# Kernel tuning notes

Measured on AMD Instinct MI355X. Metric: run time of the kernel, lower is better.

## Reference

```python
import jax, jax.numpy as jnp
import numpy as np

M, K, N = 4096, 7168, 18432  # tokens, in_features, out_features


def setup_inputs() -> dict:
    key = jax.random.key(0)
    kx, kw, ks = jax.random.split(key, 3)
    x = jax.random.normal(kx, (M, K), dtype=jnp.float32)
    # int8 quantized weight, layout [in_features, out_features] as in the torch module
    weight = jax.random.randint(kw, (K, N), -128, 128, dtype=jnp.int8)
    # per-output-channel dequant scale (bf16 in the original; fp32 here for a stable baseline)
    scale = jax.random.uniform(ks, (N,), dtype=jnp.float32) * 0.02 + 1e-3
    return {"x": x, "weight": weight, "scale": scale}


def reference(x, weight, scale):
    # Fused dequant + GEMM: y = x @ (int8_weight * scale_per_out_channel)
    w = weight.astype(x.dtype) * scale.astype(x.dtype)[None, :]  # [K, N]
    return x @ w  # [M, N]
```

## Files before the change

### kernel.cpp

```cpp
#include <hip/hip_runtime.h>
#include <hip/hip_bf16.h>
#include <cstdint>
#include <cstddef>

#define M_ 4096
#define K_ 7168
#define N_ 18432
#define NT 56

typedef __attribute__((ext_vector_type(4))) int i32x4;

#define AS1 __attribute__((address_space(1)))
#define AS3 __attribute__((address_space(3)))

__device__ __forceinline__ void gld_lds16(void* lds, const void* g) {
  __builtin_amdgcn_global_load_lds((const AS1 void*)g, (AS3 void*)lds, 16, 0, 0);
}

__global__ __launch_bounds__(256) void quant_x_kernel(const float* __restrict__ x,
                                                      signed char* __restrict__ xq,
                                                      float* __restrict__ sx) {
  const int m = blockIdx.x;
  const float4* row4 = (const float4*)(x + (size_t)m * K_);
  float mx = 0.f;
  for (int i = threadIdx.x; i < K_ / 4; i += 256) {
    float4 v = row4[i];
    mx = fmaxf(mx, fmaxf(fmaxf(fabsf(v.x), fabsf(v.y)), fmaxf(fabsf(v.z), fabsf(v.w))));
  }
#pragma unroll
  for (int d = 1; d < 64; d <<= 1) mx = fmaxf(mx, __shfl_xor(mx, d));
  __shared__ float wred[4];
  if ((threadIdx.x & 63) == 0) wred[threadIdx.x >> 6] = mx;
  __syncthreads();
  mx = fmaxf(fmaxf(wred[0], wred[1]), fmaxf(wred[2], wred[3]));
  const float inv = mx > 0.f ? 127.f / mx : 0.f;
  if (threadIdx.x == 0) sx[m] = mx / 127.f;
  char4* q4 = (char4*)(xq + (size_t)m * K_);
  for (int i = threadIdx.x; i < K_ / 4; i += 256) {
    float4 v = row4[i];
    char4 c;
    c.x = (signed char)__float2int_rn(v.x * inv);
    c.y = (signed char)__float2int_rn(v.y * inv);
    c.z = (signed char)__float2int_rn(v.z * inv);
    c.w = (signed char)__float2int_rn(v.w * inv);
    q4[i] = c;
  }
}

__global__ __launch_bounds__(256) void transpose_w_kernel(const int* __restrict__ W,
                                                          signed char* __restrict__ Wt) {
  __shared__ __align__(16) signed char t[64][80];
  const int k0 = blockIdx.x * 64;
  const int n0 = blockIdx.y * 64;
  const int r = threadIdx.x >> 4;
  const int c4 = (threadIdx.x & 15) * 4;
#pragma unroll
  for (int rr = 0; rr < 4; ++rr) {
    const int row = rr * 16 + r;
    int4 v = *(const int4*)(W + (size_t)(k0 + row) * N_ + n0 + c4);
    t[c4 + 0][row] = (signed char)v.x;
    t[c4 + 1][row] = (signed char)v.y;
    t[c4 + 2][row] = (signed char)v.z;
    t[c4 + 3][row] = (signed char)v.w;
  }
  __syncthreads();
  const int nr = threadIdx.x >> 2;
  const int cb = (threadIdx.x & 3) * 16;
  int4 o = *(const int4*)&t[nr][cb];
  *(int4*)(Wt + (size_t)(n0 + nr) * K_ + k0 + cb) = o;
}

__global__ __launch_bounds__(512, 2) void gemm_i8_kernel(const signed char* __restrict__ Aq,
                                                         const signed char* __restrict__ Bt,
                                                         const float* __restrict__ sx,
                                                         const float* __restrict__ scale,
                                                         float* __restrict__ C) {
  __shared__ __align__(16) signed char lds[131072];

  const int bid = blockIdx.x;
  const int xcd = bid & 7;
  const int j = bid >> 3;
  const int m0 = (j & 15) * 256;
  const int n0 = (xcd * 9 + (j >> 4)) * 256;

  const int tid = threadIdx.x;
  const int w = tid >> 6;
  const int lane = tid & 63;
  const int wr = w >> 2;
  const int wc = w & 3;

  const int fr = lane & 15;
  const int q = lane >> 4;
  const int sl = ((q ^ ((fr >> 1) & 3)) << 4);

  const int ls16 = (((lane & 3) ^ ((lane >> 3) & 3)) << 4);
  const int pr0 = w * 16 + (lane >> 2);
  const unsigned offA0 = (unsigned)(m0 + pr0) * K_ + ls16;
  const unsigned offA1 = (unsigned)(m0 + 128 + pr0) * K_ + ls16;
  const unsigned offB0 = (unsigned)(n0 + pr0) * K_ + ls16;
  const unsigned offB1 = (unsigned)(n0 + 128 + pr0) * K_ + ls16;

#define STAGE_A(T, KS) do {                                                        \
    const int tc_ = (T) < NT ? (T) : NT - 1;                                       \
    signed char* d_ = lds + (((T) & 1) * 32768 + (KS) * 16384 + w * 1024);         \
    gld_lds16(d_, Aq + (size_t)offA0 + tc_ * 128 + (KS) * 64);                     \
    gld_lds16(d_ + 8192, Aq + (size_t)offA1 + tc_ * 128 + (KS) * 64);              \
  } while (0)
#define STAGE_B(T, KS) do {                                                        \
    const int tc_ = (T) < NT ? (T) : NT - 1;                                       \
    signed char* d_ = lds + (65536 + ((T) & 1) * 32768 + (KS) * 16384 + w * 1024); \
    gld_lds16(d_, Bt + (size_t)offB0 + tc_ * 128 + (KS) * 64);                     \
    gld_lds16(d_ + 8192, Bt + (size_t)offB1 + tc_ * 128 + (KS) * 64);              \
  } while (0)
#define LDALL(BUF, KS) do {                                                        \
    const signed char* bb = lds + (65536 + (BUF) * 32768 + (KS) * 16384);          \
    const signed char* ab = lds + ((BUF) * 32768 + (KS) * 16384);                  \
    _Pragma("unroll") for (int n_ = 0; n_ < 4; ++n_)                               \
      fb[n_] = *(const i32x4*)(bb + (wc * 64 + n_ * 16 + fr) * 64 + sl);           \
    _Pragma("unroll") for (int f_ = 0; f_ < 8; ++f_)                               \
      fa[f_] = *(const i32x4*)(ab + (wr * 128 + f_ * 16 + fr) * 64 + sl);          \
  } while (0)
#define MFMA32 do {                                                                \
    __builtin_amdgcn_s_setprio(1);                                                 \
    _Pragma("unroll") for (int f_ = 0; f_ < 8; ++f_)                               \
    _Pragma("unroll") for (int n_ = 0; n_ < 4; ++n_)                               \
      acc[f_][n_] = __builtin_amdgcn_mfma_i32_16x16x64_i8(                         \
          fa[f_], fb[n_], acc[f_][n_], 0, 0, 0);                                   \
    __builtin_amdgcn_s_setprio(0);                                                 \
  } while (0)
#define BARRIER do { asm volatile("" ::: "memory");                                \
                     __builtin_amdgcn_s_barrier();                                 \
                     asm volatile("" ::: "memory"); } while (0)
#define WAIT00 asm volatile("s_waitcnt vmcnt(0) lgkmcnt(0)" ::: "memory")
#define VM8 asm volatile("s_waitcnt vmcnt(8)" ::: "memory")

#define KTILE(P, T_STAGE) do {                                                     \
    LDALL(P, 0);                                                                   \
    MFMA32;                                                                        \
    LDALL(P, 1);                                                                   \
    MFMA32;                                                                        \
    WAIT00;           \
    BARRIER;          \
    STAGE_A(T_STAGE, 0); STAGE_B(T_STAGE, 0);                                      \
    STAGE_A(T_STAGE, 1); STAGE_B(T_STAGE, 1);                                      \
  } while (0)

  i32x4 acc[8][4] = {};
  i32x4 fa[8], fb[4];

  STAGE_A(0, 0); STAGE_B(0, 0); STAGE_A(0, 1); STAGE_B(0, 1);
  STAGE_A(1, 0); STAGE_B(1, 0); STAGE_A(1, 1); STAGE_B(1, 1);
  VM8;
  BARRIER;

  for (int it = 0; it < NT / 2; ++it) {
    const int u = 2 * it;
    KTILE(0, u + 2);
    KTILE(1, u + 3);
  }

  const int mb = m0 + wr * 128;
  const int nb = n0 + wc * 64;
  const int col = lane & 15;
  const int rq = (lane >> 4) * 4;
  float scl[4];
#pragma unroll
  for (int n = 0; n < 4; ++n) scl[n] = scale[nb + n * 16 + col];
#pragma unroll
  for (int m = 0; m < 8; ++m) {
#pragma unroll
    for (int r = 0; r < 4; ++r) {
      const int row = mb + m * 16 + rq + r;
      const float s = sx[row];
      float* out = C + (size_t)row * N_ + nb + col;
#pragma unroll
      for (int n = 0; n < 4; ++n) out[n * 16] = (float)acc[m][n][r] * s * scl[n];
    }
  }
#undef STAGE_A
#undef STAGE_B
#undef LDALL
#undef MFMA32
#undef BARRIER
#undef WAIT00
#undef VM8
#undef KTILE
}

__global__ __launch_bounds__(256) void fb_gemm_kernel(const float* __restrict__ X,
                                                      const int* __restrict__ W,
                                                      const float* __restrict__ scale,
                                                      float* __restrict__ Y) {
  __shared__ float xs[16][65];
  __shared__ float ws_[16][65];
  const int bn = blockIdx.x * 64;
  const int bm = blockIdx.y * 64;
  const int tx = threadIdx.x & 15;
  const int ty = threadIdx.x >> 4;
  float acc[4][4] = {};
  for (int k0 = 0; k0 < K_; k0 += 16) {
    for (int i = threadIdx.x; i < 64 * 16; i += 256) {
      int r = i >> 4, c = i & 15;
      xs[c][r] = X[(size_t)(bm + r) * K_ + k0 + c];
    }
    for (int i = threadIdx.x; i < 16 * 64; i += 256) {
      int r = i >> 6, c = i & 63;
      ws_[r][c] = (float)W[(size_t)(k0 + r) * N_ + bn + c];
    }
    __syncthreads();
#pragma unroll
    for (int kk = 0; kk < 16; ++kk) {
      float a[4], b[4];
#pragma unroll
      for (int i = 0; i < 4; ++i) a[i] = xs[kk][ty * 4 + i];
#pragma unroll
      for (int j = 0; j < 4; ++j) b[j] = ws_[kk][tx * 4 + j];
#pragma unroll
      for (int i = 0; i < 4; ++i)
#pragma unroll
        for (int j = 0; j < 4; ++j) acc[i][j] += a[i] * b[j];
    }
    __syncthreads();
  }
#pragma unroll
  for (int i = 0; i < 4; ++i)
#pragma unroll
    for (int j = 0; j < 4; ++j)
      Y[(size_t)(bm + ty * 4 + i) * N_ + bn + tx * 4 + j] = acc[i][j] * scale[bn + tx * 4 + j];
}

extern "C" void kernel_launch(void* const* d_in, const int* in_sizes, int n_in,
                              void* d_out, int out_size, void* d_ws, size_t ws_size,
                              hipStream_t stream) {
  const float* x = (const float*)d_in[0];
  const int* w = (const int*)d_in[1];
  const float* scale = (const float*)d_in[2];
  float* y = (float*)d_out;

  const size_t xq_bytes = (size_t)M_ * K_;
  const size_t sx_off = xq_bytes;
  const size_t wt_off = sx_off + (size_t)M_ * 4;
  const size_t need = wt_off + (size_t)N_ * K_;

  if (ws_size >= need) {
    signed char* xq = (signed char*)d_ws;
    float* sx = (float*)((char*)d_ws + sx_off);
    signed char* wt = (signed char*)((char*)d_ws + wt_off);
    hipLaunchKernelGGL(quant_x_kernel, dim3(M_), dim3(256), 0, stream, x, xq, sx);
    hipLaunchKernelGGL(transpose_w_kernel, dim3(K_ / 64, N_ / 64), dim3(256), 0, stream, w, wt);
    hipLaunchKernelGGL(gemm_i8_kernel, dim3((M_ / 256) * (N_ / 256)), dim3(512), 0, stream,
                       xq, wt, sx, scale, y);
  } else {
    hipLaunchKernelGGL(fb_gemm_kernel, dim3(N_ / 64, M_ / 64), dim3(256), 0, stream,
                       x, w, scale, y);
  }
}
```

Before: 768.9 us.

## Switch int8 GEMM to 32x32x32 MFMA with register double-buffered fragment loads

```diff
diff --git a/kernel.cpp b/kernel.cpp
--- a/kernel.cpp
+++ b/kernel.cpp
@@ -9,6 +9,7 @@
 #define NT 56
 
 typedef __attribute__((ext_vector_type(4))) int i32x4;
+typedef __attribute__((ext_vector_type(16))) int i32x16;
 
 #define AS1 __attribute__((address_space(1)))
 #define AS3 __attribute__((address_space(3)))
@@ -89,9 +90,13 @@
   const int wr = w >> 2;
   const int wc = w & 3;
 
-  const int fr = lane & 15;
-  const int q = lane >> 4;
-  const int sl = ((q ^ ((fr >> 1) & 3)) << 4);
+  const int fr32 = lane & 31;
+  const int kh = lane >> 5;
+  const int sw = (fr32 >> 1) & 3;
+  const int ps0 = ((kh ^ sw) << 4);
+  const int ps1 = ps0 ^ 0x20;
+  const int rA = (wr * 128 + fr32) * 64;
+  const int rB = 65536 + (wc * 64 + fr32) * 64;
 
   const int ls16 = (((lane & 3) ^ ((lane >> 3) & 3)) << 4);
   const int pr0 = w * 16 + (lane >> 2);
@@ -112,46 +117,49 @@
     gld_lds16(d_, Bt + (size_t)offB0 + tc_ * 128 + (KS) * 64);                     \
     gld_lds16(d_ + 8192, Bt + (size_t)offB1 + tc_ * 128 + (KS) * 64);              \
   } while (0)
-#define LDALL(BUF, KS) do {                                                        \
-    const signed char* bb = lds + (65536 + (BUF) * 32768 + (KS) * 16384);          \
-    const signed char* ab = lds + ((BUF) * 32768 + (KS) * 16384);                  \
-    _Pragma("unroll") for (int n_ = 0; n_ < 4; ++n_)                               \
-      fb[n_] = *(const i32x4*)(bb + (wc * 64 + n_ * 16 + fr) * 64 + sl);           \
-    _Pragma("unroll") for (int f_ = 0; f_ < 8; ++f_)                               \
-      fa[f_] = *(const i32x4*)(ab + (wr * 128 + f_ * 16 + fr) * 64 + sl);          \
-  } while (0)
-#define MFMA32 do {                                                                \
+#define LDFR(FA, FB, P, KST) do {                                                  \
+    const signed char* base_ = lds + (P) * 32768 + ((KST) >> 1) * 16384            \
+                               + (((KST) & 1) ? ps1 : ps0);                        \
+    _Pragma("unroll") for (int mt_ = 0; mt_ < 4; ++mt_)                            \
+      FA[mt_] = *(const i32x4*)(base_ + rA + mt_ * 2048);                          \
+    _Pragma("unroll") for (int nt_ = 0; nt_ < 2; ++nt_)                            \
+      FB[nt_] = *(const i32x4*)(base_ + rB + nt_ * 2048);                          \
+  } while (0)
+#define MFMA8(FA, FB) do {                                                         \
     __builtin_amdgcn_s_setprio(1);                                                 \
-    _Pragma("unroll") for (int f_ = 0; f_ < 8; ++f_)                               \
-    _Pragma("unroll") for (int n_ = 0; n_ < 4; ++n_)                               \
-      acc[f_][n_] = __builtin_amdgcn_mfma_i32_16x16x64_i8(                         \
-          fa[f_], fb[n_], acc[f_][n_], 0, 0, 0);                                   \
+    _Pragma("unroll") for (int mt_ = 0; mt_ < 4; ++mt_)                            \
+    _Pragma("unroll") for (int nt_ = 0; nt_ < 2; ++nt_)                            \
+      acc[mt_][nt_] = __builtin_amdgcn_mfma_i32_32x32x32_i8(                       \
+          FA[mt_], FB[nt_], acc[mt_][nt_], 0, 0, 0);                               \
     __builtin_amdgcn_s_setprio(0);                                                 \
   } while (0)
-#define BARRIER do { asm volatile("" ::: "memory");                                \
-                     __builtin_amdgcn_s_barrier();                                 \
-                     asm volatile("" ::: "memory"); } while (0)
-#define WAIT00 asm volatile("s_waitcnt vmcnt(0) lgkmcnt(0)" ::: "memory")
+#define BAR do { asm volatile("" ::: "memory");                                    \
+                 __builtin_amdgcn_s_barrier();                                     \
+                 asm volatile("" ::: "memory"); } while (0)
+#define VM0 asm volatile("s_waitcnt vmcnt(0)" ::: "memory")
 #define VM8 asm volatile("s_waitcnt vmcnt(8)" ::: "memory")
-
-#define KTILE(P, T_STAGE) do {                                                     \
-    LDALL(P, 0);                                                                   \
-    MFMA32;                                                                        \
-    LDALL(P, 1);                                                                   \
-    MFMA32;                                                                        \
-    WAIT00;           \
-    BARRIER;          \
-    STAGE_A(T_STAGE, 0); STAGE_B(T_STAGE, 0);                                      \
-    STAGE_A(T_STAGE, 1); STAGE_B(T_STAGE, 1);                                      \
-  } while (0)
-
-  i32x4 acc[8][4] = {};
-  i32x4 fa[8], fb[4];
+#define SB __builtin_amdgcn_sched_barrier(0)
+
+#define KTILE(P, TS) do {                                                          \
+    MFMA8(fA0, fB0); LDFR(fA0, fB0, P, 2); SB;              \
+    MFMA8(fA1, fB1); LDFR(fA1, fB1, P, 3); SB;              \
+    MFMA8(fA0, fB0); SB;                                              \
+    MFMA8(fA1, fB1);                                                  \
+    VM0;            \
+    BAR;                 \
+    LDFR(fA0, fB0, (P) ^ 1, 0); LDFR(fA1, fB1, (P) ^ 1, 1); SB;                    \
+    STAGE_A(TS, 0); STAGE_B(TS, 0); STAGE_A(TS, 1); STAGE_B(TS, 1);                \
+  } while (0)
+
+  i32x16 acc[4][2] = {};
+  i32x4 fA0[4], fB0[2], fA1[4], fB1[2];
 
   STAGE_A(0, 0); STAGE_B(0, 0); STAGE_A(0, 1); STAGE_B(0, 1);
   STAGE_A(1, 0); STAGE_B(1, 0); STAGE_A(1, 1); STAGE_B(1, 1);
   VM8;
-  BARRIER;
+  BAR;
+  LDFR(fA0, fB0, 0, 0); LDFR(fA1, fB1, 0, 1);
+  SB;
 
   for (int it = 0; it < NT / 2; ++it) {
     const int u = 2 * it;
@@ -161,29 +169,29 @@
 
   const int mb = m0 + wr * 128;
   const int nb = n0 + wc * 64;
-  const int col = lane & 15;
-  const int rq = (lane >> 4) * 4;
-  float scl[4];
-#pragma unroll
-  for (int n = 0; n < 4; ++n) scl[n] = scale[nb + n * 16 + col];
-#pragma unroll
-  for (int m = 0; m < 8; ++m) {
-#pragma unroll
-    for (int r = 0; r < 4; ++r) {
-      const int row = mb + m * 16 + rq + r;
+  const int col = lane & 31;
+  const int rhi = (lane >> 5) * 4;
+  const float scl0 = scale[nb + col];
+  const float scl1 = scale[nb + 32 + col];
+#pragma unroll
+  for (int mt = 0; mt < 4; ++mt) {
+#pragma unroll
+    for (int r = 0; r < 16; ++r) {
+      const int row = mb + mt * 32 + (r & 3) + (r >> 2) * 8 + rhi;
       const float s = sx[row];
       float* out = C + (size_t)row * N_ + nb + col;
-#pragma unroll
-      for (int n = 0; n < 4; ++n) out[n * 16] = (float)acc[m][n][r] * s * scl[n];
+      out[0]  = (float)acc[mt][0][r] * s * scl0;
+      out[32] = (float)acc[mt][1][r] * s * scl1;
     }
   }
 #undef STAGE_A
 #undef STAGE_B
-#undef LDALL
-#undef MFMA32
-#undef BARRIER
-#undef WAIT00
+#undef LDFR
+#undef MFMA8
+#undef BAR
+#undef VM0
 #undef VM8
+#undef SB
 #undef KTILE
 }
 
```

Result: slower. 795.0 us (+3.4%).
